# Kernel optimization log

Hardware: AMD Instinct MI355X
Metric: run time of the kernel (lower is better)

Reference implementation:

```python
import jax, jax.numpy as jnp
import numpy as np

B, N, C, H, S = 32, 320, 768, 12, 256  # batch, tokens, dim, heads, search tokens
T = N - S  # template tokens


def setup_inputs() -> dict:
    key = jax.random.key(0)
    ks = jax.random.split(key, 8)
    w = lambda k, shape: jax.random.normal(k, shape, jnp.float32) * 0.02
    return {
        "x": jax.random.normal(ks[0], (B, N, C), jnp.float32),
        "template_mask": jax.random.uniform(ks[1], (B, T), dtype=jnp.float32),
        "qkv_w": w(ks[2], (3 * C, C)),
        "qkv_b": jnp.zeros((3 * C,), jnp.float32),
        "proj_w": w(ks[3], (C, C)),
        "proj_b": jnp.zeros((C,), jnp.float32),
        "dp1_w": w(ks[4], (384, 2 * C)),
        "dp1_b": jnp.zeros((384,), jnp.float32),
        "dp2_w": w(ks[5], (192, 384)),
        "dp2_b": jnp.zeros((192,), jnp.float32),
        "dp3_w": w(ks[6], (2, 192)),
        "dp3_b": jnp.zeros((2,), jnp.float32),
        "search_feat_len": S,
    }


def softmax_with_policy(attn, policy, eps=1e-6):
    # attn: [B,H,N,N], policy: [B,N,3]
    n = attn.shape[-1]
    p0, p1, p2 = policy[..., 0], policy[..., 1], policy[..., 2]
    # group1 + group2 + group3 (all cross terms involving group 3)
    ap = (p0[:, :, None] * p0[:, None, :]
          + p1[:, :, None] * p1[:, None, :]
          + (p0 + p1 + p2)[:, :, None] * p2[:, None, :]
          + p2[:, :, None] * (p0 + p1)[:, None, :])[:, None]  # [B,1,N,N]
    eye = jnp.eye(n, dtype=ap.dtype)
    ap = ap + (1.0 - ap) * eye
    attn = jnp.exp(attn - attn.max(axis=-1, keepdims=True)) * ap
    return (attn + eps / n) / (attn.sum(axis=-1, keepdims=True) + eps)


def reference(x, template_mask, qkv_w, qkv_b, proj_w, proj_b,
              dp1_w, dp1_b, dp2_w, dp2_b, dp3_w, dp3_b, search_feat_len):
    b, n, c = x.shape
    s = search_feat_len
    t = n - s
    h = 12
    hd = c // h
    scale = hd ** -0.5

    # tgt_type='roiavg': masked template tokens, adaptive_avg_pool1d(output_size=1)
    tgt_rep = (x[:, :t] * template_mask[:, :, None]).mean(axis=1, keepdims=True)  # [B,1,C]
    tgt_rep = jnp.broadcast_to(tgt_rep, (b, s, c))

    # divide_predict MLP (early=True): Linear(2C,384)+GELU+Linear(384,192)+GELU+Linear(192,2)+LogSoftmax
    hdn = jnp.concatenate([x[:, t:], tgt_rep], axis=-1) @ dp1_w.T + dp1_b
    hdn = jax.nn.gelu(hdn, approximate=False)
    hdn = jax.nn.gelu(hdn @ dp2_w.T + dp2_b, approximate=False)
    divide_prediction = jax.nn.log_softmax(hdn @ dp3_w.T + dp3_b, axis=-1)  # [B,S,2]

    # eval path, threshold=0, ratio=0: argmax -> one_hot decision
    decision = jax.nn.one_hot(jnp.argmax(divide_prediction, axis=-1), 2, dtype=x.dtype)  # [B,S,2]

    # policy [B,N,3]: template tokens -> group 0; search tokens -> [0, decision]
    template_policy = jnp.concatenate(
        [jnp.ones((b, t, 1), x.dtype), jnp.zeros((b, t, 2), x.dtype)], axis=-1)
    search_policy = jnp.concatenate([jnp.zeros((b, s, 1), x.dtype), decision], axis=-1)
    policy = jnp.concatenate([template_policy, search_policy], axis=1)

    qkv = (x @ qkv_w.T + qkv_b).reshape(b, n, 3, h, hd).transpose(2, 0, 3, 1, 4)
    q, k, v = qkv[0], qkv[1], qkv[2]  # [B,H,N,hd]

    attn = jnp.einsum('bhid,bhjd->bhij', q, k) * scale
    attn = softmax_with_policy(attn, policy)
    out = jnp.einsum('bhij,bhjd->bhid', attn, v)
    out = out.transpose(0, 2, 1, 3).reshape(b, n, c)
    out = out @ proj_w.T + proj_b
    return out, decision
```

## Files before the change

kernel.cpp:

```cpp
#include <hip/hip_runtime.h>
#include <hip/hip_bf16.h>

typedef unsigned short u16;
typedef unsigned int u32;
typedef unsigned long long u64;
typedef __attribute__((ext_vector_type(8))) short short8;
typedef __attribute__((ext_vector_type(4))) short s16x4;
typedef __attribute__((ext_vector_type(4))) float f32x4;

__device__ __forceinline__ float bf2f(u16 u){
  union { unsigned int i; float f; } v; v.i = ((unsigned int)u) << 16; return v.f;
}
__device__ __forceinline__ u16 f2bf(float f){
  union { float f; unsigned int i; } v; v.f = f;
  unsigned int x = v.i;
  return (u16)((x + 0x7fffu + ((x >> 16) & 1u)) >> 16);
}
__device__ __forceinline__ float gelu_exact(float x){
  return 0.5f * x * (1.0f + erff(x * 0.70710678118654752440f));
}
__device__ __forceinline__ void gld16(const void* g, void* l){
  __builtin_amdgcn_global_load_lds((const __attribute__((address_space(1))) void*)g,
                                   (__attribute__((address_space(3))) void*)l, 16, 0, 0);
}

__device__ __forceinline__ f32x4 mfma16x16x16bf16(s16x4 a, s16x4 b, f32x4 c){
#if __has_builtin(__builtin_amdgcn_mfma_f32_16x16x16_bf16)
  return __builtin_amdgcn_mfma_f32_16x16x16_bf16(a, b, c, 0, 0, 0);
#elif __has_builtin(__builtin_amdgcn_mfma_f32_16x16x16bf16_1k)
  return __builtin_amdgcn_mfma_f32_16x16x16bf16_1k(a, b, c, 0, 0, 0);
#else
  asm volatile("v_mfma_f32_16x16x16_bf16 %0, %1, %2, %3\n\ts_nop 7\n\ts_nop 3"
               : "=v"(c) : "v"(a), "v"(b), "v"(c));
  return c;
#endif
}


__global__ void k_cvt(const float* __restrict__ src, u16* __restrict__ dst, int n4){
  int i = blockIdx.x*256 + threadIdx.x;
  if (i < n4){
    float4 v = ((const float4*)src)[i];
    ushort4 p; p.x = f2bf(v.x); p.y = f2bf(v.y); p.z = f2bf(v.z); p.w = f2bf(v.w);
    ((ushort4*)dst)[i] = p;
  }
}

__global__ void k_tgt(const float* __restrict__ x, const float* __restrict__ tmask,
                      float* __restrict__ tgt){
  int b = blockIdx.x;
  int c = blockIdx.y*64 + threadIdx.x;
  float s = 0.f;
  for (int t = 0; t < 64; ++t)
    s += x[(size_t)(b*320 + t)*768 + c] * tmask[b*64 + t];
  tgt[b*768 + c] = s * (1.0f/64.0f);
}

__global__ void k_tgtdp(const float* __restrict__ tgt, const float* __restrict__ w1,
                        const float* __restrict__ b1, float* __restrict__ tgtdp){
  int b = blockIdx.x; int o = threadIdx.x;
  float s = b1[o];
  const float* wr = w1 + (size_t)o*1536 + 768;
  const float* tr = tgt + b*768;
  for (int c = 0; c < 768; ++c) s += tr[c] * wr[c];
  tgtdp[b*384 + o] = s;
}

template<int REMAP, int HASB>
__global__ __launch_bounds__(256)
void k_sgemm(const float* __restrict__ A, int lda,
             const float* __restrict__ BT, int ldb, int K,
             const float* __restrict__ bias, const float* __restrict__ tgtdp,
             float* __restrict__ out, int ldo)
{
  __shared__ float As[16][68];
  __shared__ float Bs[16][68];
  int mB = blockIdx.x*64, nB = blockIdx.y*64;
  int t = threadIdx.x;
  int tx = t & 15, ty = t >> 4;
  float acc[4][4] = {};
  for (int k0 = 0; k0 < K; k0 += 16){
    __syncthreads();
    {
      int m = t >> 2, kc = (t & 3) * 4;
      int ga = mB + m;
      if (REMAP) ga = ((ga >> 8) * 320) + 64 + (ga & 255);
      float4 av = *(const float4*)&A[(size_t)ga*lda + k0 + kc];
      As[kc+0][m] = av.x; As[kc+1][m] = av.y; As[kc+2][m] = av.z; As[kc+3][m] = av.w;
      float4 bv = *(const float4*)&BT[(size_t)(nB+m)*ldb + k0 + kc];
      Bs[kc+0][m] = bv.x; Bs[kc+1][m] = bv.y; Bs[kc+2][m] = bv.z; Bs[kc+3][m] = bv.w;
    }
    __syncthreads();
    #pragma unroll
    for (int k = 0; k < 16; ++k){
      float4 av = *(const float4*)&As[k][ty*4];
      float4 bv = *(const float4*)&Bs[k][tx*4];
      float a4[4] = {av.x, av.y, av.z, av.w};
      float b4[4] = {bv.x, bv.y, bv.z, bv.w};
      #pragma unroll
      for (int i = 0; i < 4; ++i)
        #pragma unroll
        for (int j = 0; j < 4; ++j)
          acc[i][j] += a4[i] * b4[j];
    }
  }
  #pragma unroll
  for (int i = 0; i < 4; ++i){
    int row = mB + ty*4 + i;
    #pragma unroll
    for (int j = 0; j < 4; ++j){
      int n = nB + tx*4 + j;
      float base = HASB ? bias[n] : tgtdp[(row >> 8)*384 + n];
      out[(size_t)row*ldo + n] = gelu_exact(acc[i][j] + base);
    }
  }
}

__global__ void k_decide(const float* __restrict__ h2, const float* __restrict__ w3,
                         const float* __restrict__ b3, float* __restrict__ dec,
                         unsigned char* __restrict__ gid)
{
  int t = blockIdx.x*256 + threadIdx.x;
  int b = t >> 8, s = t & 255;
  const float* hr = h2 + (size_t)t*192;
  float l0 = b3[0], l1 = b3[1];
  for (int c = 0; c < 192; ++c){
    float h = hr[c];
    l0 += h * w3[c];
    l1 += h * w3[192 + c];
  }
  int idx = (l1 > l0) ? 1 : 0;
  dec[t*2 + 0] = (idx == 0) ? 1.f : 0.f;
  dec[t*2 + 1] = (idx == 1) ? 1.f : 0.f;
  gid[b*320 + 64 + s] = (unsigned char)(2 + idx);
  if (s < 64) gid[b*320 + s] = 1;
}

template<int MODE>
__global__ __launch_bounds__(256, 2)
void k_gemm(const u16* __restrict__ A, const u16* __restrict__ BT,
            const float* __restrict__ bias, float* __restrict__ outp,
            u16* __restrict__ Qg, u16* __restrict__ Kg, u16* __restrict__ Vg)
{
  __shared__ u16 As[128*64];
  __shared__ u16 Bs[128*64];
  int mB = blockIdx.x*128, nB = blockIdx.y*128;
  int t = threadIdx.x;
  int w = t >> 6, l = t & 63;
  int wr = w >> 1, wc = w & 1;
  int lm = l & 15, lq = l >> 4;

  f32x4 zero4 = {0.f,0.f,0.f,0.f};
  f32x4 acc[4][4];
  #pragma unroll
  for (int i = 0; i < 4; ++i)
    #pragma unroll
    for (int j = 0; j < 4; ++j) acc[i][j] = zero4;

  int srow = t >> 3;
  int su0  = t & 7;
  for (int k0 = 0; k0 < 768; k0 += 64){
    __syncthreads();
    #pragma unroll
    for (int s = 0; s < 4; ++s){
      int row = s*32 + srow;
      int su  = su0 ^ (row & 7);
      gld16(&A [(size_t)(mB+row)*768 + k0 + su*8], (char*)As + s*4096 + w*1024);
      gld16(&BT[(size_t)(nB+row)*768 + k0 + su*8], (char*)Bs + s*4096 + w*1024);
    }
    __syncthreads();
    short8 af[4][2], bfv[4][2];
    #pragma unroll
    for (int mt = 0; mt < 4; ++mt){
      int r = wr*64 + mt*16 + lm;
      #pragma unroll
      for (int hh = 0; hh < 2; ++hh)
        af[mt][hh] = *(const short8*)&As[r*64 + (((hh*4 + lq) ^ (r & 7)) << 3)];
    }
    #pragma unroll
    for (int nt = 0; nt < 4; ++nt){
      int r = wc*64 + nt*16 + lm;
      #pragma unroll
      for (int hh = 0; hh < 2; ++hh)
        bfv[nt][hh] = *(const short8*)&Bs[r*64 + (((hh*4 + lq) ^ (r & 7)) << 3)];
    }
    #pragma unroll
    for (int mt = 0; mt < 4; ++mt)
      #pragma unroll
      for (int nt = 0; nt < 4; ++nt){
        acc[mt][nt] = __builtin_amdgcn_mfma_f32_16x16x32_bf16(af[mt][0], bfv[nt][0], acc[mt][nt], 0, 0, 0);
        acc[mt][nt] = __builtin_amdgcn_mfma_f32_16x16x32_bf16(af[mt][1], bfv[nt][1], acc[mt][nt], 0, 0, 0);
      }
  }

  #pragma unroll
  for (int mt = 0; mt < 4; ++mt){
    #pragma unroll
    for (int nt = 0; nt < 4; ++nt){
      int coln  = nB + wc*64 + nt*16 + lm;
      int rbase = mB + wr*64 + mt*16 + lq*4;
      float bv = bias[coln];
      if (MODE == 0){
        int bidx = rbase / 320;
        int j = rbase - bidx*320;
        if (coln >= 1536){
          int h = (coln - 1536) >> 6, d = coln & 63;
          ushort4 pk;
          pk.x = f2bf(acc[mt][nt][0] + bv);
          pk.y = f2bf(acc[mt][nt][1] + bv);
          pk.z = f2bf(acc[mt][nt][2] + bv);
          pk.w = f2bf(acc[mt][nt][3] + bv);
          *(ushort4*)&Vg[((size_t)(bidx*12 + h)*64 + d)*320 + j] = pk;
        } else {
          bool isq = coln < 768;
          int ch = isq ? coln : (coln - 768);
          int h = ch >> 6, d = ch & 63;
          u16* dst = isq ? Qg : Kg;
          #pragma unroll
          for (int r = 0; r < 4; ++r)
            dst[((size_t)(bidx*12 + h)*320 + (j + r))*64 + d] = f2bf(acc[mt][nt][r] + bv);
        }
      } else {
        #pragma unroll
        for (int r = 0; r < 4; ++r)
          outp[(size_t)(rbase + r)*768 + coln] = acc[mt][nt][r] + bv;
      }
    }
  }
}

__global__ void k_vsum(const u16* __restrict__ Vg, float* __restrict__ vsumg){
  __shared__ float vsp[4][64];
  int bh = blockIdx.x;
  int t = threadIdx.x, w = t >> 6, l = t & 63;
  const u16* vr = Vg + (size_t)bh*64*320 + (size_t)l*320 + w*80;
  float s = 0.f;
  for (int j8 = 0; j8 < 10; ++j8){
    short8 v = *(const short8*)&vr[j8*8];
    #pragma unroll
    for (int e = 0; e < 8; ++e) s += bf2f((u16)v[e]);
  }
  vsp[w][l] = s;
  __syncthreads();
  if (t < 64) vsumg[bh*64 + t] = (vsp[0][t] + vsp[1][t] + vsp[2][t] + vsp[3][t]) * (1e-6f/320.f);
}

__global__ __launch_bounds__(256, 2)
void k_attn(const u16* __restrict__ Qg, const u16* __restrict__ Kg,
            const u16* __restrict__ Vg, const unsigned char* __restrict__ gid,
            const float* __restrict__ vsumg, u16* __restrict__ aout)
{
  __shared__ u16 lds[40960];
  u16* Ks = lds;
  u16* Vs = lds + 20480;

  int g = blockIdx.x;
  int xcd = g & 7, slot = g >> 3;
  int qt = slot % 5;
  int bh = (slot / 5) * 8 + xcd;
  int b = bh / 12, h = bh % 12;
  int t = threadIdx.x, w = t >> 6, l = t & 63;
  int lm = l & 15, lq = l >> 4;
  const u16* Kbh = Kg + (size_t)bh*320*64;
  const u16* Vbh = Vg + (size_t)bh*64*320;
  const u16* Qbh = Qg + (size_t)bh*320*64;

  int qb = qt*64 + w*16;

  const u16* qp = Qbh + (size_t)(qb + lm)*64 + lq*8;
  short8 qf0 = *(const short8*)qp;
  short8 qf1 = *(const short8*)(qp + 32);
  u32 gw[20];
  #pragma unroll
  for (int jt = 0; jt < 20; ++jt)
    gw[jt] = *(const u32*)&gid[b*320 + jt*16 + lq*4];
  int gi = gid[b*320 + qb + lm];

  #pragma unroll
  for (int c = 0; c < 10; ++c){
    int base = (w*10 + c) * 1024;
    int off  = base + l*16;
    int r  = off >> 7;
    int u  = (off >> 4) & 7;
    const u16* src = Kbh + r*64 + ((u ^ (r & 7)) << 3);
    gld16(src, (char*)Ks + base);
  }
  #pragma unroll
  for (int c = 0; c < 10; ++c){
    int base = (w*10 + c) * 1024;
    int off  = base + l*16;
    int d    = off / 640;
    int uu   = (off - d*640) >> 4;
    const u16* src = Vbh + d*320 + ((uu ^ (d & 7)) << 3);
    gld16(src, (char*)Vs + base);
  }
  __syncthreads();

  const float cexp = 0.125f * 1.44269504088896340736f;
  f32x4 zero4 = {0.f,0.f,0.f,0.f};
  int swz = lm & 7;

  const u16* kb0 = Ks + lm*64 + (((lq    ) ^ swz) << 3);
  const u16* kb1 = Ks + lm*64 + (((lq + 4) ^ swz) << 3);
  f32x4 sacc[20];
  #pragma unroll
  for (int jt = 0; jt < 20; ++jt){
    short8 kf0 = *(const short8*)(kb0 + jt*1024);
    short8 kf1 = *(const short8*)(kb1 + jt*1024);
    f32x4 a = zero4;
    a = __builtin_amdgcn_mfma_f32_16x16x32_bf16(kf0, qf0, a, 0, 0, 0);
    a = __builtin_amdgcn_mfma_f32_16x16x32_bf16(kf1, qf1, a, 0, 0, 0);
    sacc[jt] = a;
  }
  float m = -3.402823466e+38f;
  #pragma unroll
  for (int jt = 0; jt < 20; ++jt)
    m = fmaxf(m, fmaxf(fmaxf(sacc[jt][0], sacc[jt][1]),
                       fmaxf(sacc[jt][2], sacc[jt][3])));
  m = fmaxf(m, __shfl_xor(m, 16, 64));
  m = fmaxf(m, __shfl_xor(m, 32, 64));

  bool gin3 = (gi != 3);
  float sm = 0.f;
  f32x4 oacc[4];
  #pragma unroll
  for (int nt = 0; nt < 4; ++nt) oacc[nt] = zero4;
  const u16* vb = Vs + lm*320 + ((lq & 1) << 2);

  #pragma unroll
  for (int jt = 0; jt < 20; ++jt){
    u32 gwj = gw[jt];
    float e0, e1, e2, e3;
    {
      float ev = exp2f((sacc[jt][0] - m) * cexp);
      u32 gj = gwj & 255u;
      if (gin3 && (gj != 3u) && ((u32)gi != gj)) ev = 0.f;
      sm += ev; e0 = ev;
    }
    {
      float ev = exp2f((sacc[jt][1] - m) * cexp);
      u32 gj = (gwj >> 8) & 255u;
      if (gin3 && (gj != 3u) && ((u32)gi != gj)) ev = 0.f;
      sm += ev; e1 = ev;
    }
    {
      float ev = exp2f((sacc[jt][2] - m) * cexp);
      u32 gj = (gwj >> 16) & 255u;
      if (gin3 && (gj != 3u) && ((u32)gi != gj)) ev = 0.f;
      sm += ev; e2 = ev;
    }
    {
      float ev = exp2f((sacc[jt][3] - m) * cexp);
      u32 gj = gwj >> 24;
      if (gin3 && (gj != 3u) && ((u32)gi != gj)) ev = 0.f;
      sm += ev; e3 = ev;
    }
    u32 w0, w1;
    asm("v_cvt_pk_bf16_f32 %0, %1, %2" : "=v"(w0) : "v"(e0), "v"(e1));
    asm("v_cvt_pk_bf16_f32 %0, %1, %2" : "=v"(w1) : "v"(e2), "v"(e3));
    union { u32 u[2]; s16x4 v; } pu;
    pu.u[0] = w0; pu.u[1] = w1;
    s16x4 pa = pu.v;
    int vu = (((2*jt + (lq >> 1)) ^ swz) << 3);
    #pragma unroll
    for (int nt = 0; nt < 4; ++nt){
      s16x4 vf = *(const s16x4*)(vb + vu + nt*5120);
      oacc[nt] = mfma16x16x16bf16(pa, vf, oacc[nt]);
    }
  }
  sm += __shfl_xor(sm, 16, 64);
  sm += __shfl_xor(sm, 32, 64);
  float inv = 1.0f / (sm + 1e-6f);
  float invO[4];
  #pragma unroll
  for (int r = 0; r < 4; ++r) invO[r] = __shfl(inv, lq*4 + r, 64);

  #pragma unroll
  for (int nt = 0; nt < 4; ++nt){
    int d = nt*16 + lm;
    float vs = vsumg[bh*64 + d];
    #pragma unroll
    for (int r = 0; r < 4; ++r){
      int row = qt*64 + w*16 + lq*4 + r;
      float v = (oacc[nt][r] + vs) * invO[r];
      aout[(size_t)(b*320 + row)*768 + h*64 + d] = f2bf(v);
    }
  }
}

extern "C" void kernel_launch(void* const* d_in, const int* in_sizes, int n_in,
                              void* d_out, int out_size, void* d_ws, size_t ws_size,
                              hipStream_t stream)
{
  const float* x      = (const float*)d_in[0];
  const float* tmask  = (const float*)d_in[1];
  const float* qkv_w  = (const float*)d_in[2];
  const float* qkv_b  = (const float*)d_in[3];
  const float* proj_w = (const float*)d_in[4];
  const float* proj_b = (const float*)d_in[5];
  const float* dp1_w  = (const float*)d_in[6];
  const float* dp1_b  = (const float*)d_in[7];
  const float* dp2_w  = (const float*)d_in[8];
  const float* dp2_b  = (const float*)d_in[9];
  const float* dp3_w  = (const float*)d_in[10];
  const float* dp3_b  = (const float*)d_in[11];

  char* ws = (char*)d_ws;
  float* tgt    = (float*)(ws + 0);
  float* tgtdp  = (float*)(ws + 98304);
  float* h1     = (float*)(ws + 147456);
  float* h2     = (float*)(ws + 12730368);
  unsigned char* gid = (unsigned char*)(ws + 19021824);
  u16* xb     = (u16*)(ws + 19032064);
  u16* qkvwb  = (u16*)(ws + 34760704);
  u16* projwb = (u16*)(ws + 38299648);
  u16* Qg     = (u16*)(ws + 39479296);
  u16* Kg     = (u16*)(ws + 55207936);
  u16* Vg     = (u16*)(ws + 70936576);
  u16* aout   = (u16*)(ws + 147456);
  float* vsumg = (float*)(ws + 18923520);

  float* out = (float*)d_out;
  float* dec = out + 7864320;

  hipLaunchKernelGGL(k_cvt, dim3(7680), dim3(256), 0, stream, x, xb, 1966080);
  hipLaunchKernelGGL(k_cvt, dim3(1728), dim3(256), 0, stream, qkv_w, qkvwb, 442368);
  hipLaunchKernelGGL(k_cvt, dim3(576),  dim3(256), 0, stream, proj_w, projwb, 147456);
  hipLaunchKernelGGL(k_tgt,   dim3(32, 12), dim3(64), 0, stream, x, tmask, tgt);
  hipLaunchKernelGGL(k_tgtdp, dim3(32), dim3(384), 0, stream, tgt, dp1_w, dp1_b, tgtdp);
  hipLaunchKernelGGL((k_sgemm<1,0>), dim3(128, 6), dim3(256), 0, stream,
                     x, 768, dp1_w, 1536, 768, (const float*)nullptr, tgtdp, h1, 384);
  hipLaunchKernelGGL((k_sgemm<0,1>), dim3(128, 3), dim3(256), 0, stream,
                     h1, 384, dp2_w, 384, 384, dp2_b, (const float*)nullptr, h2, 192);
  hipLaunchKernelGGL(k_decide, dim3(32), dim3(256), 0, stream, h2, dp3_w, dp3_b, dec, gid);
  hipLaunchKernelGGL((k_gemm<0>), dim3(80, 18), dim3(256), 0, stream,
                     xb, qkvwb, qkv_b, (float*)nullptr, Qg, Kg, Vg);
  hipLaunchKernelGGL(k_vsum, dim3(384), dim3(256), 0, stream, Vg, vsumg);
  hipLaunchKernelGGL(k_attn, dim3(1920), dim3(256), 0, stream, Qg, Kg, Vg, gid, vsumg, aout);
  hipLaunchKernelGGL((k_gemm<1>), dim3(80, 6), dim3(256), 0, stream,
                     aout, projwb, proj_b, out, (u16*)nullptr, (u16*)nullptr, (u16*)nullptr);
}
```

Before: 374.9 us.

## Merge conversion kernels and co-schedule dp1 SGEMM with QKV GEMM

```diff
diff --git a/kernel.cpp b/kernel.cpp
--- a/kernel.cpp
+++ b/kernel.cpp
@@ -37,13 +37,17 @@
 }
 
 
-__global__ void k_cvt(const float* __restrict__ src, u16* __restrict__ dst, int n4){
-  int i = blockIdx.x*256 + threadIdx.x;
-  if (i < n4){
-    float4 v = ((const float4*)src)[i];
-    ushort4 p; p.x = f2bf(v.x); p.y = f2bf(v.y); p.z = f2bf(v.z); p.w = f2bf(v.w);
-    ((ushort4*)dst)[i] = p;
-  }
+__global__ void k_cvt3(const float* __restrict__ s0, u16* __restrict__ d0,
+                       const float* __restrict__ s1, u16* __restrict__ d1,
+                       const float* __restrict__ s2, u16* __restrict__ d2){
+  int bx = blockIdx.x;
+  const float* src; u16* dst; int i;
+  if (bx < 7680){ src = s0; dst = d0; i = bx*256 + threadIdx.x; }
+  else if (bx < 9408){ src = s1; dst = d1; i = (bx - 7680)*256 + threadIdx.x; }
+  else { src = s2; dst = d2; i = (bx - 9408)*256 + threadIdx.x; }
+  float4 v = ((const float4*)src)[i];
+  ushort4 p; p.x = f2bf(v.x); p.y = f2bf(v.y); p.z = f2bf(v.z); p.w = f2bf(v.w);
+  ((ushort4*)dst)[i] = p;
 }
 
 __global__ void k_tgt(const float* __restrict__ x, const float* __restrict__ tmask,
@@ -64,6 +68,139 @@
   const float* tr = tgt + b*768;
   for (int c = 0; c < 768; ++c) s += tr[c] * wr[c];
   tgtdp[b*384 + o] = s;
+}
+
+__global__ __launch_bounds__(256, 2)
+void k_fused1(const float* __restrict__ A, const float* __restrict__ BT,
+              const float* __restrict__ tgtdp, float* __restrict__ h1,
+              const u16* __restrict__ GA, const u16* __restrict__ GB,
+              const float* __restrict__ bias,
+              u16* __restrict__ Qg, u16* __restrict__ Kg, u16* __restrict__ Vg)
+{
+  __shared__ char smem[32768];
+  int bx = blockIdx.x;
+  int t = threadIdx.x;
+  if (bx < 768){
+    float (*As)[68] = (float(*)[68])smem;
+    float (*Bs)[68] = (float(*)[68])(smem + 4352);
+    int mB = (bx & 127)*64, nB = (bx >> 7)*64;
+    int tx = t & 15, ty = t >> 4;
+    float acc[4][4] = {};
+    for (int k0 = 0; k0 < 768; k0 += 16){
+      __syncthreads();
+      {
+        int m = t >> 2, kc = (t & 3) * 4;
+        int ga = mB + m;
+        ga = ((ga >> 8) * 320) + 64 + (ga & 255);
+        float4 av = *(const float4*)&A[(size_t)ga*768 + k0 + kc];
+        As[kc+0][m] = av.x; As[kc+1][m] = av.y; As[kc+2][m] = av.z; As[kc+3][m] = av.w;
+        float4 bv = *(const float4*)&BT[(size_t)(nB+m)*1536 + k0 + kc];
+        Bs[kc+0][m] = bv.x; Bs[kc+1][m] = bv.y; Bs[kc+2][m] = bv.z; Bs[kc+3][m] = bv.w;
+      }
+      __syncthreads();
+      #pragma unroll
+      for (int k = 0; k < 16; ++k){
+        float4 av = *(const float4*)&As[k][ty*4];
+        float4 bv = *(const float4*)&Bs[k][tx*4];
+        float a4[4] = {av.x, av.y, av.z, av.w};
+        float b4[4] = {bv.x, bv.y, bv.z, bv.w};
+        #pragma unroll
+        for (int i = 0; i < 4; ++i)
+          #pragma unroll
+          for (int j = 0; j < 4; ++j)
+            acc[i][j] += a4[i] * b4[j];
+      }
+    }
+    #pragma unroll
+    for (int i = 0; i < 4; ++i){
+      int row = mB + ty*4 + i;
+      #pragma unroll
+      for (int j = 0; j < 4; ++j){
+        int n = nB + tx*4 + j;
+        float base = tgtdp[(row >> 8)*384 + n];
+        h1[(size_t)row*384 + n] = gelu_exact(acc[i][j] + base);
+      }
+    }
+  } else {
+    u16* As = (u16*)smem;
+    u16* Bs = (u16*)(smem + 16384);
+    int i2 = bx - 768;
+    int mB = (i2 % 80)*128, nB = (i2 / 80)*128;
+    int w = t >> 6, l = t & 63;
+    int wr = w >> 1, wc = w & 1;
+    int lm = l & 15, lq = l >> 4;
+
+    f32x4 zero4 = {0.f,0.f,0.f,0.f};
+    f32x4 acc[4][4];
+    #pragma unroll
+    for (int i = 0; i < 4; ++i)
+      #pragma unroll
+      for (int j = 0; j < 4; ++j) acc[i][j] = zero4;
+
+    int srow = t >> 3;
+    int su0  = t & 7;
+    for (int k0 = 0; k0 < 768; k0 += 64){
+      __syncthreads();
+      #pragma unroll
+      for (int s = 0; s < 4; ++s){
+        int row = s*32 + srow;
+        int su  = su0 ^ (row & 7);
+        gld16(&GA[(size_t)(mB+row)*768 + k0 + su*8], (char*)As + s*4096 + w*1024);
+        gld16(&GB[(size_t)(nB+row)*768 + k0 + su*8], (char*)Bs + s*4096 + w*1024);
+      }
+      __syncthreads();
+      short8 af[4][2], bfv[4][2];
+      #pragma unroll
+      for (int mt = 0; mt < 4; ++mt){
+        int r = wr*64 + mt*16 + lm;
+        #pragma unroll
+        for (int hh = 0; hh < 2; ++hh)
+          af[mt][hh] = *(const short8*)&As[r*64 + (((hh*4 + lq) ^ (r & 7)) << 3)];
+      }
+      #pragma unroll
+      for (int nt = 0; nt < 4; ++nt){
+        int r = wc*64 + nt*16 + lm;
+        #pragma unroll
+        for (int hh = 0; hh < 2; ++hh)
+          bfv[nt][hh] = *(const short8*)&Bs[r*64 + (((hh*4 + lq) ^ (r & 7)) << 3)];
+      }
+      #pragma unroll
+      for (int mt = 0; mt < 4; ++mt)
+        #pragma unroll
+        for (int nt = 0; nt < 4; ++nt){
+          acc[mt][nt] = __builtin_amdgcn_mfma_f32_16x16x32_bf16(af[mt][0], bfv[nt][0], acc[mt][nt], 0, 0, 0);
+          acc[mt][nt] = __builtin_amdgcn_mfma_f32_16x16x32_bf16(af[mt][1], bfv[nt][1], acc[mt][nt], 0, 0, 0);
+        }
+    }
+    #pragma unroll
+    for (int mt = 0; mt < 4; ++mt){
+      #pragma unroll
+      for (int nt = 0; nt < 4; ++nt){
+        int coln  = nB + wc*64 + nt*16 + lm;
+        int rbase = mB + wr*64 + mt*16 + lq*4;
+        float bv = bias[coln];
+        int bidx = rbase / 320;
+        int j = rbase - bidx*320;
+        if (coln >= 1536){
+          int h = (coln - 1536) >> 6, d = coln & 63;
+          ushort4 pk;
+          pk.x = f2bf(acc[mt][nt][0] + bv);
+          pk.y = f2bf(acc[mt][nt][1] + bv);
+          pk.z = f2bf(acc[mt][nt][2] + bv);
+          pk.w = f2bf(acc[mt][nt][3] + bv);
+          *(ushort4*)&Vg[((size_t)(bidx*12 + h)*64 + d)*320 + j] = pk;
+        } else {
+          bool isq = coln < 768;
+          int ch = isq ? coln : (coln - 768);
+          int h = ch >> 6, d = ch & 63;
+          u16* dst = isq ? Qg : Kg;
+          #pragma unroll
+          for (int r = 0; r < 4; ++r)
+            dst[((size_t)(bidx*12 + h)*320 + (j + r))*64 + d] = f2bf(acc[mt][nt][r] + bv);
+        }
+      }
+    }
+  }
 }
 
 template<int REMAP, int HASB>
@@ -423,18 +560,15 @@
   float* out = (float*)d_out;
   float* dec = out + 7864320;
 
-  hipLaunchKernelGGL(k_cvt, dim3(7680), dim3(256), 0, stream, x, xb, 1966080);
-  hipLaunchKernelGGL(k_cvt, dim3(1728), dim3(256), 0, stream, qkv_w, qkvwb, 442368);
-  hipLaunchKernelGGL(k_cvt, dim3(576),  dim3(256), 0, stream, proj_w, projwb, 147456);
+  hipLaunchKernelGGL(k_cvt3, dim3(9984), dim3(256), 0, stream,
+                     x, xb, qkv_w, qkvwb, proj_w, projwb);
   hipLaunchKernelGGL(k_tgt,   dim3(32, 12), dim3(64), 0, stream, x, tmask, tgt);
   hipLaunchKernelGGL(k_tgtdp, dim3(32), dim3(384), 0, stream, tgt, dp1_w, dp1_b, tgtdp);
-  hipLaunchKernelGGL((k_sgemm<1,0>), dim3(128, 6), dim3(256), 0, stream,
-                     x, 768, dp1_w, 1536, 768, (const float*)nullptr, tgtdp, h1, 384);
+  hipLaunchKernelGGL(k_fused1, dim3(2208), dim3(256), 0, stream,
+                     x, dp1_w, tgtdp, h1, xb, qkvwb, qkv_b, Qg, Kg, Vg);
   hipLaunchKernelGGL((k_sgemm<0,1>), dim3(128, 3), dim3(256), 0, stream,
                      h1, 384, dp2_w, 384, 384, dp2_b, (const float*)nullptr, h2, 192);
   hipLaunchKernelGGL(k_decide, dim3(32), dim3(256), 0, stream, h2, dp3_w, dp3_b, dec, gid);
-  hipLaunchKernelGGL((k_gemm<0>), dim3(80, 18), dim3(256), 0, stream,
-                     xb, qkvwb, qkv_b, (float*)nullptr, Qg, Kg, Vg);
   hipLaunchKernelGGL(k_vsum, dim3(384), dim3(256), 0, stream, Vg, vsumg);
   hipLaunchKernelGGL(k_attn, dim3(1920), dim3(256), 0, stream, Qg, Kg, Vg, gid, vsumg, aout);
   hipLaunchKernelGGL((k_gemm<1>), dim3(80, 6), dim3(256), 0, stream,
```

Result: faster. 358.6 us (-4.3%).
